# Kernel tuning notes

Hardware: AMD Instinct MI355X
Metric: run time of the kernel (lower is better)

The kernel has to match this reference:

```python
import jax, jax.numpy as jnp
import numpy as np

B, S, D = 2, 4096, 1024
H, DK, DV = 4, 128, 256          # head_k_dim, head_v_dim
KD, VD = H * DK, H * DV          # key_dim=512, value_dim=1024
RANK = 16                        # gate_low_rank_dim
GLN = 16.0                       # gate_logit_normalizer
EPS = 1e-5
C = 64                           # chunk size
NC = S // C


def setup_inputs() -> dict:
    key = jax.random.key(0)
    ks = jax.random.split(key, 9)
    w = lambda k, shape: (jax.random.normal(k, shape, jnp.float32) * 0.02)
    return {
        "x": jax.random.normal(ks[0], (B, S, D), jnp.float32),
        "Wq": w(ks[1], (D, KD)),
        "Wk": w(ks[2], (D, KD)),
        "Wv": w(ks[3], (D, VD)),
        "Wgk1": w(ks[4], (D, RANK)),
        "Wgk2": w(ks[5], (RANK, KD)),
        "bgk": jnp.zeros((KD,), jnp.float32),
        "Wg": w(ks[6], (D, VD)),
        "Wo": w(ks[7], (VD, D)),
        "norm_w": jnp.ones((DV,), jnp.float32),
    }


def _gla_chunk(q, k, v, gk):
    """Chunkwise gated linear attention. q,k,gk: [B,S,H,DK]; v: [B,S,H,DV]."""
    qc = q.reshape(B, NC, C, H, DK)
    kc = k.reshape(B, NC, C, H, DK)
    vc = v.reshape(B, NC, C, H, DV)
    gc = gk.reshape(B, NC, C, H, DK)
    gcum = jnp.cumsum(gc, axis=2)                       # inclusive within-chunk cumsum (<= 0)
    g_last = gcum[:, :, -1]                             # [B,NC,H,DK]
    q_t = qc * jnp.exp(gcum)                            # q decayed forward
    k_inv = kc * jnp.exp(-gcum)                         # for intra-chunk scores
    k_dec = kc * jnp.exp(g_last[:, :, None] - gcum)     # for state update (bounded)
    # intra-chunk causal scores
    A = jnp.einsum('bnthk,bnshk->bnhts', q_t, k_inv)    # [B,NC,H,C,C]
    mask = jnp.tril(jnp.ones((C, C), bool))
    A = jnp.where(mask, A, 0.0)
    o_intra = jnp.einsum('bnhts,bnshv->bnthv', A, vc)   # [B,NC,C,H,DV]
    # per-chunk state contribution
    kv = jnp.einsum('bnthk,bnthv->bnhkv', k_dec, vc)    # [B,NC,H,DK,DV]

    def step(state, inp):
        q_tc, gl, kvc = inp                             # [B,C,H,DK], [B,H,DK], [B,H,DK,DV]
        o_inter = jnp.einsum('bthk,bhkv->bthv', q_tc, state)
        state = state * jnp.exp(gl)[..., None] + kvc
        return state, o_inter

    xs = (jnp.swapaxes(q_t, 0, 1), jnp.swapaxes(g_last, 0, 1), jnp.swapaxes(kv, 0, 1))
    init = jnp.zeros((B, H, DK, DV), q.dtype)
    _, o_inter = jax.lax.scan(step, init, xs)           # [NC,B,C,H,DV]
    o = o_intra + jnp.swapaxes(o_inter, 0, 1)
    return o.reshape(B, S, H, DV)


def reference(x, Wq, Wk, Wv, Wgk1, Wgk2, bgk, Wg, Wo, norm_w):
    scale = DK ** -0.5
    q = (x @ Wq).reshape(B, S, H, DK) * scale
    k = (x @ Wk).reshape(B, S, H, DK)
    v = (x @ Wv).reshape(B, S, H, DV)
    gk = (jax.nn.log_sigmoid((x @ Wgk1) @ Wgk2 + bgk) / GLN).reshape(B, S, H, DK)
    o = _gla_chunk(q, k, v, gk)                          # [B,S,H,DV]
    # fused RMSNorm + swish gate (per-head norm over DV)
    g = (x @ Wg).reshape(B, S, H, DV)
    o = o * jax.lax.rsqrt(jnp.mean(o * o, axis=-1, keepdims=True) + EPS) * norm_w
    o = o * (g * jax.nn.sigmoid(g))
    return o.reshape(B, S, VD) @ Wo
```

## Files before the change

### kernel.cpp

```cpp
#include <hip/hip_runtime.h>

typedef __bf16 bf16_t;
typedef __bf16 bf16x8 __attribute__((ext_vector_type(8)));
typedef float  f32x4  __attribute__((ext_vector_type(4)));

#define MFMA16(a,b,c) __builtin_amdgcn_mfma_f32_16x16x32_bf16((a),(b),(c),0,0,0)

#define SCALE_Q 0.08838834764831845f

#define GLOBAL_LOAD_LDS16(gptr, lptr)                                          \
  __builtin_amdgcn_global_load_lds(                                            \
      (const __attribute__((address_space(1))) void*)(gptr),                   \
      (__attribute__((address_space(3))) void*)(lptr), 16, 0, 0)

__global__ __launch_bounds__(256) void k_convert(const void* __restrict__ src,
                                                 const unsigned int* __restrict__ nwp,
                                                 bf16_t* __restrict__ dst, int n) {
  bool isf32 = (nwp[0] == 0x3F800000u);
  int g = blockIdx.x * 256 + threadIdx.x;
  int i = g * 8;
  if (i >= n) return;
  if (isf32) {
    const float4* s = (const float4*)src;
    float4 a = s[g * 2], b = s[g * 2 + 1];
    bf16x8 o;
    o[0] = (bf16_t)a.x; o[1] = (bf16_t)a.y; o[2] = (bf16_t)a.z; o[3] = (bf16_t)a.w;
    o[4] = (bf16_t)b.x; o[5] = (bf16_t)b.y; o[6] = (bf16_t)b.z; o[7] = (bf16_t)b.w;
    *(bf16x8*)(dst + i) = o;
  } else {
    *(bf16x8*)(dst + i) = ((const bf16x8*)src)[g];
  }
}

struct ConvSrcs {
  const void *wq, *wk, *wv, *wg, *wo, *gk1, *gk2, *bgk, *nw;
};
__device__ __forceinline__ void convT_tile(const void* src, bf16_t* dst,
                                           int Ccols, int bx, int by,
                                           bool isf32, bf16_t (*t)[33]) {
  int tx = threadIdx.x & 31, ty = threadIdx.x >> 5;
  int r0 = by * 32, c0 = bx * 32;
#pragma unroll
  for (int i = 0; i < 4; i++) {
    int r = r0 + ty + i * 8, cc = c0 + tx;
    float v = isf32 ? ((const float*)src)[(size_t)r * Ccols + cc]
                    : (float)((const bf16_t*)src)[(size_t)r * Ccols + cc];
    t[ty + i * 8][tx] = (bf16_t)v;
  }
  __syncthreads();
#pragma unroll
  for (int i = 0; i < 4; i++) {
    int cc = c0 + ty + i * 8;
    dst[(size_t)cc * 1024 + r0 + tx] = t[tx][ty + i * 8];
  }
}
__device__ __forceinline__ void conv_straight(const void* src, bf16_t* dst,
                                              int base_blk, int n, bool isf32) {
  int g = (blockIdx.x - base_blk) * 256 + threadIdx.x;
  int i = g * 8;
  if (i >= n) return;
  if (isf32) {
    const float4* s = (const float4*)src;
    float4 a = s[g * 2], b = s[g * 2 + 1];
    bf16x8 o;
    o[0] = (bf16_t)a.x; o[1] = (bf16_t)a.y; o[2] = (bf16_t)a.z; o[3] = (bf16_t)a.w;
    o[4] = (bf16_t)b.x; o[5] = (bf16_t)b.y; o[6] = (bf16_t)b.z; o[7] = (bf16_t)b.w;
    *(bf16x8*)(dst + i) = o;
  } else {
    *(bf16x8*)(dst + i) = ((const bf16x8*)src)[g];
  }
}
__global__ __launch_bounds__(256) void k_convW(ConvSrcs s,
                                               const unsigned int* __restrict__ nwp,
                                               bf16_t* __restrict__ tWcat,
                                               bf16_t* __restrict__ tWo,
                                               bf16_t* __restrict__ cWgk1,
                                               bf16_t* __restrict__ cWgk2,
                                               bf16_t* __restrict__ cbgk,
                                               bf16_t* __restrict__ cnw) {
  __shared__ bf16_t t[32][33];
  bool isf32 = (nwp[0] == 0x3F800000u);
  int blk = blockIdx.x;
  if (blk < 512) {
    convT_tile(s.wq, tWcat, 512, blk & 15, blk >> 4, isf32, t);
  } else if (blk < 1024) {
    int b2 = blk - 512;
    convT_tile(s.wk, tWcat + (size_t)512 * 1024, 512, b2 & 15, b2 >> 4, isf32, t);
  } else if (blk < 2048) {
    int b2 = blk - 1024;
    convT_tile(s.wv, tWcat + (size_t)1024 * 1024, 1024, b2 & 31, b2 >> 5, isf32, t);
  } else if (blk < 3072) {
    int b2 = blk - 2048;
    convT_tile(s.wg, tWcat + (size_t)2048 * 1024, 1024, b2 & 31, b2 >> 5, isf32, t);
  } else if (blk < 4096) {
    int b2 = blk - 3072;
    convT_tile(s.wo, tWo, 1024, b2 & 31, b2 >> 5, isf32, t);
  } else if (blk < 4104) {
    conv_straight(s.gk1, cWgk1, 4096, 16384, isf32);
  } else if (blk < 4108) {
    conv_straight(s.gk2, cWgk2, 4104, 8192, isf32);
  } else if (blk == 4108) {
    conv_straight(s.bgk, cbgk, 4108, 512, isf32);
  } else {
    conv_straight(s.nw, cnw, 4109, 256, isf32);
  }
}

__global__ __launch_bounds__(256) void k_gk1(const bf16_t* __restrict__ x,
                                             const bf16_t* __restrict__ W1,
                                             float* __restrict__ tmp) {
  int wave = threadIdx.x >> 6, lane = threadIdx.x & 63;
  int m = blockIdx.x * 4 + wave;
  const bf16_t* xr = x + (size_t)m * 1024;
  float p[16];
#pragma unroll
  for (int n = 0; n < 16; n++) p[n] = 0.f;
  for (int kk = 0; kk < 16; kk++) {
    int k = kk * 64 + lane;
    float xv = (float)xr[k];
    bf16x8 w0 = *(const bf16x8*)(W1 + k * 16);
    bf16x8 w1 = *(const bf16x8*)(W1 + k * 16 + 8);
#pragma unroll
    for (int j = 0; j < 8; j++) {
      p[j]     += xv * (float)w0[j];
      p[8 + j] += xv * (float)w1[j];
    }
  }
#pragma unroll
  for (int off = 1; off < 64; off <<= 1) {
#pragma unroll
    for (int n = 0; n < 16; n++) p[n] += __shfl_xor(p[n], off, 64);
  }
#pragma unroll
  for (int n = 0; n < 16; n++)
    if (lane == n) tmp[(size_t)m * 16 + n] = p[n];
}

__global__ __launch_bounds__(256) void k_gk2(const float* __restrict__ tmp,
                                             const bf16_t* __restrict__ W2,
                                             const bf16_t* __restrict__ bgk,
                                             float* __restrict__ gcum) {
  int g = blockIdx.x * 256 + threadIdx.x;
  int m = g >> 6;
  int n0 = (g & 63) * 8;
  float acc[8];
#pragma unroll
  for (int j = 0; j < 8; j++) acc[j] = 0.f;
  for (int k = 0; k < 16; k++) {
    float tv = tmp[(size_t)m * 16 + k];
    bf16x8 w = *(const bf16x8*)(W2 + k * 512 + n0);
#pragma unroll
    for (int j = 0; j < 8; j++) acc[j] += tv * (float)w[j];
  }
  int b = m >> 12, s = m & 4095;
  int h = n0 >> 7, dk0 = n0 & 127;
  float* dst = gcum + (((size_t)(b * 4 + h) * 4096 + s) * 128 + dk0);
#pragma unroll
  for (int j = 0; j < 8; j++) {
    float z = acc[j] + (float)bgk[n0 + j];
    float lg = -__logf(1.f + __expf(-z)) * (1.f / 16.f);
    dst[j] = fmaxf(lg, -4.0f);
  }
}

__global__ __launch_bounds__(128) void k_cumsum(float* __restrict__ gcum,
                                                float* __restrict__ glast) {
  int blk = blockIdx.x;
  int dk = threadIdx.x;
  float* base = gcum + (size_t)blk * 8192;
  float run = 0.f;
  for (int t = 0; t < 64; t++) {
    run += base[t * 128 + dk];
    base[t * 128 + dk] = run;
  }
  glast[(size_t)blk * 128 + dk] = run;
}

__global__ __launch_bounds__(256, 4) void k_gemm(const bf16_t* __restrict__ Ag,
                                              const bf16_t* __restrict__ Bt,
                                              int mode,
                                              const float* __restrict__ gcum,
                                              const float* __restrict__ glast,
                                              bf16_t* __restrict__ qt,
                                              bf16_t* __restrict__ kinv,
                                              bf16_t* __restrict__ kdec,
                                              bf16_t* __restrict__ vr,
                                              bf16_t* __restrict__ gmat,
                                              float* __restrict__ fout) {
  __shared__ __attribute__((aligned(16))) bf16_t As[2 * 128 * 32];
  __shared__ __attribute__((aligned(16))) bf16_t Bs[2 * 128 * 32];
  int tid = threadIdx.x;
  int wave = tid >> 6, lane = tid & 63, quad = lane >> 4, c = lane & 15;
  int m0 = blockIdx.y * 128, n0 = blockIdx.x * 128;
  int wm = (wave >> 1) * 64, wn = (wave & 1) * 64;
  int r0s = wave * 32 + (lane >> 2);
  int r1s = r0s + 16;
  int s = lane & 3;
  int f0 = (s - (r0s >> 1)) & 3;
  int f1 = (s - (r1s >> 1)) & 3;
  const bf16_t* a0 = Ag + (size_t)(m0 + r0s) * 1024 + f0 * 8;
  const bf16_t* a1 = Ag + (size_t)(m0 + r1s) * 1024 + f1 * 8;
  const bf16_t* b0 = Bt + (size_t)(n0 + r0s) * 1024 + f0 * 8;
  const bf16_t* b1 = Bt + (size_t)(n0 + r1s) * 1024 + f1 * 8;
  bf16_t* lA = As + wave * 1024;
  bf16_t* lB = Bs + wave * 1024;
  int raOff[4], rbOff[4];
#pragma unroll
  for (int t4 = 0; t4 < 4; t4++) {
    int ra = wm + t4 * 16 + c;
    raOff[t4] = ra * 32 + (((quad + (ra >> 1)) & 3) * 8);
    int rb = wn + t4 * 16 + c;
    rbOff[t4] = rb * 32 + (((quad + (rb >> 1)) & 3) * 8);
  }
  GLOBAL_LOAD_LDS16(a0, lA);
  GLOBAL_LOAD_LDS16(a1, lA + 512);
  GLOBAL_LOAD_LDS16(b0, lB);
  GLOBAL_LOAD_LDS16(b1, lB + 512);
  f32x4 acc[4][4] = {};
  for (int k0 = 0; k0 < 1024; k0 += 32) {
    __syncthreads();
    int cur = (k0 >> 5) & 1;
    int nxtoff = (cur ^ 1) * 4096;
    if (k0 + 32 < 1024) {
      GLOBAL_LOAD_LDS16(a0 + k0 + 32, lA + nxtoff);
      GLOBAL_LOAD_LDS16(a1 + k0 + 32, lA + nxtoff + 512);
      GLOBAL_LOAD_LDS16(b0 + k0 + 32, lB + nxtoff);
      GLOBAL_LOAD_LDS16(b1 + k0 + 32, lB + nxtoff + 512);
    }
    int curoff = cur * 4096;
    bf16x8 af[4], bfr[4];
#pragma unroll
    for (int t4 = 0; t4 < 4; t4++) af[t4] = *(const bf16x8*)(As + curoff + raOff[t4]);
#pragma unroll
    for (int t4 = 0; t4 < 4; t4++) bfr[t4] = *(const bf16x8*)(Bs + curoff + rbOff[t4]);
#pragma unroll
    for (int mt = 0; mt < 4; mt++)
#pragma unroll
      for (int nt = 0; nt < 4; nt++)
        acc[mt][nt] = MFMA16(af[mt], bfr[nt], acc[mt][nt]);
  }
#pragma unroll
  for (int mt = 0; mt < 4; mt++)
#pragma unroll
    for (int nt = 0; nt < 4; nt++)
#pragma unroll
      for (int r = 0; r < 4; r++) {
        int m = m0 + wm + mt * 16 + quad * 4 + r;
        int n = n0 + wn + nt * 16 + c;
        float v = acc[mt][nt][r];
        if (mode == 1) {
          fout[(size_t)m * 1024 + n] = v;
        } else if (n0 < 512) {
          int b = m >> 12, ss = m & 4095, h = n >> 7, dk = n & 127;
          size_t idx = ((size_t)(b * 4 + h) * 4096 + ss) * 128 + dk;
          qt[idx] = (bf16_t)(v * SCALE_Q * __expf(gcum[idx]));
        } else if (n0 < 1024) {
          int nk = n - 512;
          int b = m >> 12, ss = m & 4095, h = nk >> 7, dk = nk & 127;
          size_t idx = ((size_t)(b * 4 + h) * 4096 + ss) * 128 + dk;
          float gc = gcum[idx];
          float gl = glast[((size_t)(b * 4 + h) * 64 + (ss >> 6)) * 128 + dk];
          kinv[idx] = (bf16_t)(v * __expf(fminf(-gc, 30.f)));
          kdec[idx] = (bf16_t)(v * __expf(gl - gc));
        } else if (n0 < 2048) {
          int nv = n - 1024;
          int b = m >> 12, ss = m & 4095, h = nv >> 8, dv = nv & 255;
          vr[((size_t)(b * 4 + h) * 4096 + ss) * 256 + dv] = (bf16_t)v;
        } else {
          gmat[(size_t)m * 1024 + (n - 2048)] = (bf16_t)v;
        }
      }
}

__global__ __launch_bounds__(256) void k_attA(const bf16_t* __restrict__ qt,
                                              const bf16_t* __restrict__ kinv,
                                              bf16_t* __restrict__ Aout) {
  int blk = blockIdx.x;
  size_t cb = (size_t)blk * 8192;
  int tid = threadIdx.x, wave = tid >> 6, lane = tid & 63;
  int quad = lane >> 4, c = lane & 15;
  f32x4 acc[4] = {};
  for (int kk = 0; kk < 128; kk += 32) {
    bf16x8 a = *(const bf16x8*)(qt + cb + (size_t)(wave * 16 + c) * 128 + kk + quad * 8);
#pragma unroll
    for (int nt = 0; nt < 4; nt++) {
      bf16x8 bb = *(const bf16x8*)(kinv + cb + (size_t)(nt * 16 + c) * 128 + kk + quad * 8);
      acc[nt] = MFMA16(a, bb, acc[nt]);
    }
  }
#pragma unroll
  for (int nt = 0; nt < 4; nt++)
#pragma unroll
    for (int r = 0; r < 4; r++) {
      int row = wave * 16 + quad * 4 + r, col = nt * 16 + c;
      Aout[(size_t)blk * 4096 + row * 64 + col] =
          (bf16_t)(col <= row ? acc[nt][r] : 0.f);
    }
}

__global__ __launch_bounds__(256, 3) void k_kv(const bf16_t* __restrict__ kdec,
                                            const bf16_t* __restrict__ vr,
                                            bf16_t* __restrict__ kv) {
  int blk = blockIdx.x;
  __shared__ __attribute__((aligned(16))) bf16_t ls_kd[64 * 128];
  __shared__ __attribute__((aligned(16))) bf16_t ls_v[64 * 256];
  int tid = threadIdx.x, wave = tid >> 6, lane = tid & 63;
  int quad = lane >> 4, c = lane & 15;
  size_t cb = (size_t)blk * 8192;
  size_t cv = (size_t)blk * 16384;
  size_t sb = (size_t)blk * 32768;
#pragma unroll
  for (int j = 0; j < 4; j++) {
    int idx = tid + j * 256;
    int row = idx >> 4, col = (idx & 15) * 8;
    *(bf16x8*)&ls_kd[row * 128 + col] = *(const bf16x8*)(kdec + cb + (size_t)row * 128 + col);
  }
#pragma unroll
  for (int j = 0; j < 8; j++) {
    int idx = tid + j * 256;
    int row = idx >> 5, col = (idx & 31) * 8;
    *(bf16x8*)&ls_v[row * 256 + col] = *(const bf16x8*)(vr + cv + (size_t)row * 256 + col);
  }
  __syncthreads();
  int kbase = (wave >> 1) * 64;
  for (int pos = 0; pos < 2; pos++) {
    int dvbase = (wave & 1) * 64 + pos * 128;
    f32x4 acc[4][4] = {};
    for (int kk = 0; kk < 64; kk += 32) {
      bf16x8 a[4], bb[4];
#pragma unroll
      for (int mt = 0; mt < 4; mt++)
#pragma unroll
        for (int j = 0; j < 8; j++)
          a[mt][j] = ls_kd[(kk + quad * 8 + j) * 128 + kbase + mt * 16 + c];
#pragma unroll
      for (int nt = 0; nt < 4; nt++)
#pragma unroll
        for (int j = 0; j < 8; j++)
          bb[nt][j] = ls_v[(kk + quad * 8 + j) * 256 + dvbase + nt * 16 + c];
#pragma unroll
      for (int mt = 0; mt < 4; mt++)
#pragma unroll
        for (int nt = 0; nt < 4; nt++)
          acc[mt][nt] = MFMA16(a[mt], bb[nt], acc[mt][nt]);
    }
#pragma unroll
    for (int mt = 0; mt < 4; mt++)
#pragma unroll
      for (int nt = 0; nt < 4; nt++)
#pragma unroll
        for (int r = 0; r < 4; r++) {
          int kg = kbase + mt * 16 + quad * 4 + r;
          int dg = dvbase + nt * 16 + c;
          kv[sb + (size_t)kg * 256 + dg] = (bf16_t)acc[mt][nt][r];
        }
  }
}

__global__ __launch_bounds__(256) void k_scan2(bf16_t* __restrict__ states,
                                               const float* __restrict__ glast) {
  int g = blockIdx.x * 256 + threadIdx.x;
  int bh = g >> 15;
  int idx = g & 32767;
  int kg = idx >> 8;
  bf16_t* p = states + (size_t)bh * 64 * 32768 + idx;
  const float* gl = glast + (size_t)bh * 64 * 128 + kg;
  float carry = 0.f;
#pragma unroll 4
  for (int n = 0; n < 64; n++) {
    float kvv = (float)p[(size_t)n * 32768];
    float e = __expf(gl[n * 128]);
    p[(size_t)n * 32768] = (bf16_t)carry;
    carry = carry * e + kvv;
  }
}

__global__ __launch_bounds__(256, 4) void k_o(const bf16_t* __restrict__ qt,
                                           const bf16_t* __restrict__ Amat,
                                           const bf16_t* __restrict__ vr,
                                           const bf16_t* __restrict__ states,
                                           const bf16_t* __restrict__ gmat,
                                           const bf16_t* __restrict__ normw,
                                           bf16_t* __restrict__ ob) {
  int blk = blockIdx.x;
  int bh = blk >> 6, n = blk & 63, b = bh >> 2, h = bh & 3;
  __shared__ __attribute__((aligned(16))) bf16_t ls[64 * 256];
  __shared__ __attribute__((aligned(16))) float lred[64][4];
  int tid = threadIdx.x, wave = tid >> 6, lane = tid & 63;
  int quad = lane >> 4, c = lane & 15;
  size_t cb = (size_t)blk * 8192;
  size_t cv = (size_t)blk * 16384;
  size_t sb = (size_t)blk * 32768;
  f32x4 acc[4][4] = {};
  for (int half = 0; half < 2; half++) {
    __syncthreads();
#pragma unroll
    for (int i = 0; i < 8; i++) {
      int idx = tid + i * 256;
      int row = idx >> 5, col = (idx & 31) * 8;
      *(bf16x8*)&ls[row * 256 + col] =
          *(const bf16x8*)(states + sb + (size_t)(half * 64 + row) * 256 + col);
    }
    __syncthreads();
    for (int kk2 = 0; kk2 < 2; kk2++) {
      int kl = kk2 * 32, kg = half * 64 + kl;
      bf16x8 a[4], bb[4];
#pragma unroll
      for (int mt = 0; mt < 4; mt++)
        a[mt] = *(const bf16x8*)(qt + cb + (size_t)(mt * 16 + c) * 128 + kg + quad * 8);
#pragma unroll
      for (int nt = 0; nt < 4; nt++)
#pragma unroll
        for (int j = 0; j < 8; j++)
          bb[nt][j] = ls[(kl + quad * 8 + j) * 256 + wave * 64 + nt * 16 + c];
#pragma unroll
      for (int mt = 0; mt < 4; mt++)
#pragma unroll
        for (int nt = 0; nt < 4; nt++)
          acc[mt][nt] = MFMA16(a[mt], bb[nt], acc[mt][nt]);
    }
  }
  __syncthreads();
#pragma unroll
  for (int i = 0; i < 8; i++) {
    int idx = tid + i * 256;
    int row = idx >> 5, col = (idx & 31) * 8;
    *(bf16x8*)&ls[row * 256 + col] =
        *(const bf16x8*)(vr + cv + (size_t)row * 256 + col);
  }
  __syncthreads();
  for (int kk = 0; kk < 64; kk += 32) {
    bf16x8 a[4], bb[4];
#pragma unroll
    for (int mt = 0; mt < 4; mt++)
      a[mt] = *(const bf16x8*)(Amat + (size_t)blk * 4096 + (size_t)(mt * 16 + c) * 64 + kk + quad * 8);
#pragma unroll
    for (int nt = 0; nt < 4; nt++)
#pragma unroll
      for (int j = 0; j < 8; j++)
        bb[nt][j] = ls[(kk + quad * 8 + j) * 256 + wave * 64 + nt * 16 + c];
#pragma unroll
    for (int mt = 0; mt < 4; mt++)
#pragma unroll
      for (int nt = 0; nt < 4; nt++)
        acc[mt][nt] = MFMA16(a[mt], bb[nt], acc[mt][nt]);
  }
  float p[4][4];
#pragma unroll
  for (int mt = 0; mt < 4; mt++)
#pragma unroll
    for (int r = 0; r < 4; r++) {
      float s = 0.f;
#pragma unroll
      for (int nt = 0; nt < 4; nt++) s += acc[mt][nt][r] * acc[mt][nt][r];
      p[mt][r] = s;
    }
#pragma unroll
  for (int off = 1; off < 16; off <<= 1) {
#pragma unroll
    for (int mt = 0; mt < 4; mt++)
#pragma unroll
      for (int r = 0; r < 4; r++) p[mt][r] += __shfl_xor(p[mt][r], off, 64);
  }
  if (c == 0) {
#pragma unroll
    for (int mt = 0; mt < 4; mt++)
#pragma unroll
      for (int r = 0; r < 4; r++) lred[mt * 16 + quad * 4 + r][wave] = p[mt][r];
  }
  __syncthreads();
#pragma unroll
  for (int mt = 0; mt < 4; mt++)
#pragma unroll
    for (int r = 0; r < 4; r++) {
      int row = mt * 16 + quad * 4 + r;
      float tot = lred[row][0] + lred[row][1] + lred[row][2] + lred[row][3];
      float rs = rsqrtf(tot * (1.f / 256.f) + 1e-5f);
      int sg = n * 64 + row;
      size_t gb = ((size_t)(b * 4096 + sg)) * 1024 + h * 256;
#pragma unroll
      for (int nt = 0; nt < 4; nt++) {
        int dv = wave * 64 + nt * 16 + c;
        float ov = acc[mt][nt][r] * rs * (float)normw[dv];
        float gv = (float)gmat[gb + dv];
        ov *= gv / (1.f + __expf(-gv));
        ob[gb + dv] = (bf16_t)ov;
      }
    }
}

extern "C" void kernel_launch(void* const* d_in, const int* in_sizes, int n_in,
                              void* d_out, int out_size, void* d_ws, size_t ws_size,
                              hipStream_t stream) {
  (void)in_sizes; (void)n_in; (void)out_size; (void)ws_size;
  const unsigned int* nw_oracle = (const unsigned int*)d_in[9];

  char* ws = (char*)d_ws;
  size_t off = 0;
  auto alloc = [&](size_t bytes) -> void* {
    void* p = ws + off;
    off += (bytes + 255) & ~(size_t)255;
    return p;
  };
  bf16_t* states = (bf16_t*)alloc((size_t)512 * 32768 * 2);
  bf16_t* cx     = states;
  float*  glast  = (float*) alloc((size_t)8 * 64 * 128 * 4);
  float*  tmp    = (float*) alloc((size_t)8192 * 16 * 4);
  float*  gcum   = (float*) alloc((size_t)8 * 4096 * 128 * 4);
  bf16_t* ob     = (bf16_t*)gcum;
  bf16_t* qt     = (bf16_t*)alloc((size_t)8 * 4096 * 128 * 2);
  bf16_t* kinv   = (bf16_t*)alloc((size_t)8 * 4096 * 128 * 2);
  bf16_t* kdec   = (bf16_t*)alloc((size_t)8 * 4096 * 128 * 2);
  bf16_t* vr     = (bf16_t*)alloc((size_t)8 * 4096 * 256 * 2);
  bf16_t* gmat   = (bf16_t*)alloc((size_t)8192 * 1024 * 2);
  bf16_t* Amat   = (bf16_t*)alloc((size_t)512 * 4096 * 2);
  bf16_t* tWcat  = (bf16_t*)alloc((size_t)3072 * 1024 * 2);
  bf16_t* cWgk1  = (bf16_t*)alloc((size_t)1024 * 16 * 2);
  bf16_t* cWgk2  = (bf16_t*)alloc((size_t)16 * 512 * 2);
  bf16_t* cbgk   = (bf16_t*)alloc((size_t)512 * 2);
  bf16_t* tWo    = (bf16_t*)alloc((size_t)1024 * 1024 * 2);
  bf16_t* cnw    = (bf16_t*)alloc((size_t)256 * 2);

  k_convert<<<4096, 256, 0, stream>>>(d_in[0], nw_oracle, cx, 8192 * 1024);
  ConvSrcs cs{d_in[1], d_in[2], d_in[3], d_in[7], d_in[8],
              d_in[4], d_in[5], d_in[6], d_in[9]};
  k_convW<<<4110, 256, 0, stream>>>(cs, nw_oracle, tWcat, tWo,
                                    cWgk1, cWgk2, cbgk, cnw);

  k_gk1<<<2048, 256, 0, stream>>>(cx, cWgk1, tmp);
  k_gk2<<<2048, 256, 0, stream>>>(tmp, cWgk2, cbgk, gcum);
  k_cumsum<<<512, 128, 0, stream>>>(gcum, glast);
  k_gemm<<<dim3(24, 64), 256, 0, stream>>>(cx, tWcat, 0, gcum, glast,
                                           qt, kinv, kdec, vr, gmat, nullptr);
  k_attA<<<512, 256, 0, stream>>>(qt, kinv, Amat);
  k_kv<<<512, 256, 0, stream>>>(kdec, vr, states);
  k_scan2<<<1024, 256, 0, stream>>>(states, glast);
  k_o<<<512, 256, 0, stream>>>(qt, Amat, vr, states, gmat, cnw, ob);
  k_gemm<<<dim3(8, 64), 256, 0, stream>>>(ob, tWo, 1, nullptr, nullptr,
                                          nullptr, nullptr, nullptr, nullptr, nullptr,
                                          (float*)d_out);
}
```

Baseline: 345.4 us.

## Load GEMM operands directly from global into registers, dropping LDS staging

The main GEMM kernel no longer stages A and B tiles through LDS with global_load_lds and barriers. Each wave now loads its own MFMA fragments straight from global memory into double-buffered registers, prefetching the next K-slice. This removes LDS traffic and __syncthreads, but loses cross-wave sharing: each A/B row is fetched by both waves that use it, so the kernel relies on L1/L2 for reuse. The loads are also less coalesced (16-byte per-lane strided rows). The launch bound drops occupancy to 3 blocks to make room for the extra registers.

```diff
diff --git a/kernel.cpp b/kernel.cpp
--- a/kernel.cpp
+++ b/kernel.cpp
@@ -7,11 +7,6 @@
 #define MFMA16(a,b,c) __builtin_amdgcn_mfma_f32_16x16x32_bf16((a),(b),(c),0,0,0)
 
 #define SCALE_Q 0.08838834764831845f
-
-#define GLOBAL_LOAD_LDS16(gptr, lptr)                                          \
-  __builtin_amdgcn_global_load_lds(                                            \
-      (const __attribute__((address_space(1))) void*)(gptr),                   \
-      (__attribute__((address_space(3))) void*)(lptr), 16, 0, 0)
 
 __global__ __launch_bounds__(256) void k_convert(const void* __restrict__ src,
                                                  const unsigned int* __restrict__ nwp,
@@ -176,7 +171,7 @@
   glast[(size_t)blk * 128 + dk] = run;
 }
 
-__global__ __launch_bounds__(256, 4) void k_gemm(const bf16_t* __restrict__ Ag,
+__global__ __launch_bounds__(256, 3) void k_gemm(const bf16_t* __restrict__ Ag,
                                               const bf16_t* __restrict__ Bt,
                                               int mode,
                                               const float* __restrict__ gcum,
@@ -187,57 +182,39 @@
                                               bf16_t* __restrict__ vr,
                                               bf16_t* __restrict__ gmat,
                                               float* __restrict__ fout) {
-  __shared__ __attribute__((aligned(16))) bf16_t As[2 * 128 * 32];
-  __shared__ __attribute__((aligned(16))) bf16_t Bs[2 * 128 * 32];
   int tid = threadIdx.x;
   int wave = tid >> 6, lane = tid & 63, quad = lane >> 4, c = lane & 15;
   int m0 = blockIdx.y * 128, n0 = blockIdx.x * 128;
   int wm = (wave >> 1) * 64, wn = (wave & 1) * 64;
-  int r0s = wave * 32 + (lane >> 2);
-  int r1s = r0s + 16;
-  int s = lane & 3;
-  int f0 = (s - (r0s >> 1)) & 3;
-  int f1 = (s - (r1s >> 1)) & 3;
-  const bf16_t* a0 = Ag + (size_t)(m0 + r0s) * 1024 + f0 * 8;
-  const bf16_t* a1 = Ag + (size_t)(m0 + r1s) * 1024 + f1 * 8;
-  const bf16_t* b0 = Bt + (size_t)(n0 + r0s) * 1024 + f0 * 8;
-  const bf16_t* b1 = Bt + (size_t)(n0 + r1s) * 1024 + f1 * 8;
-  bf16_t* lA = As + wave * 1024;
-  bf16_t* lB = Bs + wave * 1024;
-  int raOff[4], rbOff[4];
+  const bf16_t* ap[4];
+  const bf16_t* bp[4];
 #pragma unroll
   for (int t4 = 0; t4 < 4; t4++) {
-    int ra = wm + t4 * 16 + c;
-    raOff[t4] = ra * 32 + (((quad + (ra >> 1)) & 3) * 8);
-    int rb = wn + t4 * 16 + c;
-    rbOff[t4] = rb * 32 + (((quad + (rb >> 1)) & 3) * 8);
-  }
-  GLOBAL_LOAD_LDS16(a0, lA);
-  GLOBAL_LOAD_LDS16(a1, lA + 512);
-  GLOBAL_LOAD_LDS16(b0, lB);
-  GLOBAL_LOAD_LDS16(b1, lB + 512);
+    ap[t4] = Ag + (size_t)(m0 + wm + t4 * 16 + c) * 1024 + quad * 8;
+    bp[t4] = Bt + (size_t)(n0 + wn + t4 * 16 + c) * 1024 + quad * 8;
+  }
+  bf16x8 af[2][4], bfr[2][4];
+#pragma unroll
+  for (int t4 = 0; t4 < 4; t4++) {
+    af[0][t4] = *(const bf16x8*)(ap[t4]);
+    bfr[0][t4] = *(const bf16x8*)(bp[t4]);
+  }
   f32x4 acc[4][4] = {};
-  for (int k0 = 0; k0 < 1024; k0 += 32) {
-    __syncthreads();
-    int cur = (k0 >> 5) & 1;
-    int nxtoff = (cur ^ 1) * 4096;
-    if (k0 + 32 < 1024) {
-      GLOBAL_LOAD_LDS16(a0 + k0 + 32, lA + nxtoff);
-      GLOBAL_LOAD_LDS16(a1 + k0 + 32, lA + nxtoff + 512);
-      GLOBAL_LOAD_LDS16(b0 + k0 + 32, lB + nxtoff);
-      GLOBAL_LOAD_LDS16(b1 + k0 + 32, lB + nxtoff + 512);
-    }
-    int curoff = cur * 4096;
-    bf16x8 af[4], bfr[4];
-#pragma unroll
-    for (int t4 = 0; t4 < 4; t4++) af[t4] = *(const bf16x8*)(As + curoff + raOff[t4]);
-#pragma unroll
-    for (int t4 = 0; t4 < 4; t4++) bfr[t4] = *(const bf16x8*)(Bs + curoff + rbOff[t4]);
+#pragma unroll 2
+  for (int it = 0; it < 32; it++) {
+    int cur = it & 1, nxt = cur ^ 1;
+    if (it < 31) {
+#pragma unroll
+      for (int t4 = 0; t4 < 4; t4++) {
+        af[nxt][t4] = *(const bf16x8*)(ap[t4] + (it + 1) * 32);
+        bfr[nxt][t4] = *(const bf16x8*)(bp[t4] + (it + 1) * 32);
+      }
+    }
 #pragma unroll
     for (int mt = 0; mt < 4; mt++)
 #pragma unroll
       for (int nt = 0; nt < 4; nt++)
-        acc[mt][nt] = MFMA16(af[mt], bfr[nt], acc[mt][nt]);
+        acc[mt][nt] = MFMA16(af[cur][mt], bfr[cur][nt], acc[mt][nt]);
   }
 #pragma unroll
   for (int mt = 0; mt < 4; mt++)
```

New measurement: 499.7 us. 44.7% more time.
